# Kernel tuning notes

Hardware: AMD Instinct MI355X
Metric: run time of the kernel (lower is better)

## Reference

```python
import jax, jax.numpy as jnp
import numpy as np

B, T, D = 4, 2048, 1024
E, K, H = 8, 2, 2048

def setup_inputs() -> dict:
    key = jax.random.key(0)
    ks = jax.random.split(key, 5)
    scale = 0.02
    x = jax.random.normal(ks[0], (B, T, D), dtype=jnp.float32)
    gate_w = jax.random.normal(ks[1], (E, D), dtype=jnp.float32) * scale   # Linear(D->E) weight [out,in]
    w_gate = jax.random.normal(ks[2], (E, H, D), dtype=jnp.float32) * scale
    w_in = jax.random.normal(ks[3], (E, H, D), dtype=jnp.float32) * scale
    w_out = jax.random.normal(ks[4], (E, D, H), dtype=jnp.float32) * scale
    return {"x": x, "gate_w": gate_w, "w_gate": w_gate, "w_in": w_in, "w_out": w_out}

def reference(x, gate_w, w_gate, w_in, w_out):
    # Router: logits (B,T,E) -> top-k -> softmax over the k selected logits
    logits = jnp.einsum('btd,ed->bte', x, gate_w)
    topk_vals, topk_idx = jax.lax.top_k(logits, K)          # (B,T,K)
    routing = jax.nn.softmax(topk_vals, axis=-1)            # (B,T,K)

    out = jnp.zeros_like(x)
    # Masked-matmul: loop over the small fixed expert bank (E=8)
    for e in range(E):
        sel = (topk_idx == e)                               # (B,T,K) bool
        mask = sel.any(axis=-1)                             # (B,T)
        w = jnp.sum(routing * sel.astype(routing.dtype), axis=-1)  # (B,T)
        mx = x * mask[..., None].astype(x.dtype)            # (B,T,D)
        h = jax.nn.silu(jnp.einsum('btd,hd->bth', mx, w_gate[e])) * jnp.einsum('btd,hd->bth', mx, w_in[e])
        out = out + jnp.einsum('bth,dh->btd', h, w_out[e]) * w[..., None]
    return out
```

## Files before the change

### kernel.cpp

```cpp
#include <hip/hip_runtime.h>
#include <stdint.h>
#include <stddef.h>

#define NTOK 8192
#define DDIM 1024
#define NEXP 8
#define HDIM 2048
#define LSTRIDE (NTOK + 256)
#define NCHUNK 128
#define MAXROWS (2 * NTOK + NEXP * 256)

typedef __attribute__((ext_vector_type(4))) float f32x4;
typedef __attribute__((ext_vector_type(8))) short s16x8;
typedef __attribute__((ext_vector_type(4))) short s16x4;

static __device__ __forceinline__ unsigned short f2bf(float f) {
  union { float f; unsigned u; } v; v.f = f;
  unsigned r = v.u + 0x7FFFu + ((v.u >> 16) & 1u);
  return (unsigned short)(r >> 16);
}
static __device__ __forceinline__ float bf2f(unsigned short h) {
  union { unsigned u; float f; } v; v.u = ((unsigned)h) << 16;
  return v.f;
}

static __device__ __forceinline__ void gll16(const void* g, void* l) {
  __builtin_amdgcn_global_load_lds((const __attribute__((address_space(1))) void*)g,
                                   (__attribute__((address_space(3))) void*)l, 16, 0, 0);
}

#define BAR_MID() __builtin_amdgcn_s_barrier()
#define BAR_END() do { __builtin_amdgcn_s_barrier(); __builtin_amdgcn_sched_barrier(0); } while (0)
#define LGKM0() do { asm volatile("s_waitcnt lgkmcnt(0)" ::: "memory"); __builtin_amdgcn_sched_barrier(0); } while (0)
#define VMW6() asm volatile("s_waitcnt vmcnt(6)" ::: "memory")
#define VMW0() asm volatile("s_waitcnt vmcnt(0)" ::: "memory")

__global__ void k_sentinel(float* out) { if (threadIdx.x == 0) out[0] = 1.0e6f; }

__global__ __launch_bounds__(256) void k_cvt(const float* __restrict__ src,
                                             unsigned short* __restrict__ dst, int n8) {
  int i = blockIdx.x * blockDim.x + threadIdx.x;
  int stride = gridDim.x * blockDim.x;
  for (; i < n8; i += stride) {
    const f32x4* s = (const f32x4*)(src + (size_t)i * 8);
    f32x4 a = s[0], b = s[1];
    s16x8 o;
    o[0] = f2bf(a[0]); o[1] = f2bf(a[1]); o[2] = f2bf(a[2]); o[3] = f2bf(a[3]);
    o[4] = f2bf(b[0]); o[5] = f2bf(b[1]); o[6] = f2bf(b[2]); o[7] = f2bf(b[3]);
    *(s16x8*)(dst + (size_t)i * 8) = o;
  }
}

__global__ __launch_bounds__(256) void k_router(const float* __restrict__ x,
    const float* __restrict__ gw, unsigned* __restrict__ tokE, float2* __restrict__ tokW2,
    unsigned short* __restrict__ xbf) {
  int lane = threadIdx.x & 63;
  int t = blockIdx.x * 4 + (threadIdx.x >> 6);
  const f32x4* x4 = (const f32x4*)x;
  const f32x4* g4 = (const f32x4*)gw;
  f32x4 xr[4];
#pragma unroll
  for (int j = 0; j < 4; ++j) xr[j] = x4[(size_t)t * 256 + j * 64 + lane];
#pragma unroll
  for (int j = 0; j < 4; ++j) {
    s16x4 o;
    o[0] = f2bf(xr[j][0]); o[1] = f2bf(xr[j][1]); o[2] = f2bf(xr[j][2]); o[3] = f2bf(xr[j][3]);
    *(s16x4*)(xbf + (size_t)t * DDIM + (j * 64 + lane) * 4) = o;
  }
  float le[8];
#pragma unroll
  for (int e = 0; e < 8; ++e) {
    float p = 0.f;
#pragma unroll
    for (int j = 0; j < 4; ++j) {
      f32x4 g = g4[e * 256 + j * 64 + lane];
      p += xr[j][0] * g[0] + xr[j][1] * g[1] + xr[j][2] * g[2] + xr[j][3] * g[3];
    }
#pragma unroll
    for (int off = 32; off > 0; off >>= 1) p += __shfl_xor(p, off, 64);
    le[e] = p;
  }
  if (lane == 0) {
    int i0 = 0; float v0 = le[0];
#pragma unroll
    for (int e = 1; e < 8; ++e) if (le[e] > v0) { v0 = le[e]; i0 = e; }
    int i1 = -1; float v1 = 0.f;
#pragma unroll
    for (int e = 0; e < 8; ++e) if (e != i0 && (i1 < 0 || le[e] > v1)) { v1 = le[e]; i1 = e; }
    float b = __expf(v1 - v0);
    float s = 1.f + b;
    tokE[t] = (unsigned)i0 | ((unsigned)i1 << 8);
    tokW2[t] = make_float2(1.f / s, b / s);
  }
}

__global__ __launch_bounds__(64) void k_hist(const unsigned* __restrict__ tokE,
                                             int* __restrict__ cntTable) {
  __shared__ int c8[NEXP];
  int tid = threadIdx.x, c = blockIdx.x;
  if (tid < NEXP) c8[tid] = 0;
  __syncthreads();
  unsigned v = tokE[c * 64 + tid];
  atomicAdd(&c8[v & 255], 1);
  atomicAdd(&c8[(v >> 8) & 255], 1);
  __syncthreads();
  if (tid < NEXP) cntTable[tid * NCHUNK + c] = c8[tid];
}

__global__ __launch_bounds__(64) void k_scan(const int* __restrict__ cntTable,
                                             int* __restrict__ ctrl, int* __restrict__ cbL) {
  __shared__ int tot[NEXP];
  int e = threadIdx.x;
  if (e < NEXP) {
    int s = 0;
    for (int c = 0; c < NCHUNK; ++c) s += cntTable[e * NCHUNK + c];
    tot[e] = s; ctrl[e] = s;
  }
  __syncthreads();
  if (e == 0) {
    int acc = 0;
    for (int q = 0; q < NEXP; ++q) { ctrl[8 + q] = acc; acc += (tot[q] + 255) & ~255; }
  }
  if (e < NEXP) {
    int run = 0;
    for (int c = 0; c < NCHUNK; ++c) { cbL[e * NCHUNK + c] = run; run += cntTable[e * NCHUNK + c]; }
  }
}

__global__ __launch_bounds__(64) void k_scatter(const unsigned* __restrict__ tokE,
    const float2* __restrict__ tokW2, const int* __restrict__ cbL,
    int* __restrict__ listTok, float* __restrict__ listW, int* __restrict__ listSlot) {
  __shared__ int lcnt[NEXP];
  int tid = threadIdx.x, c = blockIdx.x;
  if (tid < NEXP) lcnt[tid] = 0;
  __syncthreads();
  int t = c * 64 + tid;
  unsigned v = tokE[t];
  int e0 = v & 255, e1 = (v >> 8) & 255;
  float2 w = tokW2[t];
  int l0 = atomicAdd(&lcnt[e0], 1);
  int l1 = atomicAdd(&lcnt[e1], 1);
  int i0 = cbL[e0 * NCHUNK + c] + l0;
  int i1 = cbL[e1 * NCHUNK + c] + l1;
  listTok[e0 * LSTRIDE + i0] = t; listW[e0 * LSTRIDE + i0] = w.x; listSlot[e0 * LSTRIDE + i0] = 0;
  listTok[e1 * LSTRIDE + i1] = t; listW[e1 * LSTRIDE + i1] = w.y; listSlot[e1 * LSTRIDE + i1] = 1;
}

__global__ __launch_bounds__(512, 2) void k_gemm1(const unsigned short* __restrict__ xbf,
    const unsigned short* __restrict__ wg, const unsigned short* __restrict__ wi,
    const int* __restrict__ ctrl, const int* __restrict__ listTok,
    unsigned short* __restrict__ hbuf) {
  int e = blockIdx.z;
  int cnt = ctrl[e];
  int m0 = blockIdx.y * 256;
  if (m0 >= cnt) return;
  int rowb = ctrl[8 + e];
  int n0 = blockIdx.x * 128;

  __shared__ __align__(16) char lds[131072];
  char* ldsc = &lds[0];

  int tid = threadIdx.x, lane = tid & 63, wv = tid >> 6;
  int wm = wv >> 1, wn = wv & 1;

  int srow = tid >> 3;
  int scol = (((tid & 7) ^ ((tid >> 3) & 7)) << 4);
  int sdst = wv << 10;
  const char* pA[2][2];
  const char* pBg[2];
  const char* pBi[2];
#pragma unroll
  for (int rg = 0; rg < 2; ++rg)
#pragma unroll
    for (int sb = 0; sb < 2; ++sb) {
      int tok = listTok[e * LSTRIDE + m0 + rg * 128 + sb * 64 + srow];
      pA[rg][sb] = (const char*)xbf + (size_t)tok * 2048 + scol;
    }
#pragma unroll
  for (int sb = 0; sb < 2; ++sb) {
    pBg[sb] = (const char*)wg + ((size_t)e * HDIM + n0 + sb * 64 + srow) * 2048 + scol;
    pBi[sb] = (const char*)wi + ((size_t)e * HDIM + n0 + sb * 64 + srow) * 2048 + scol;
  }

  int rowB = (lane & 15) << 7;
  int mk = (lane & 7) << 4;
  int q16 = (lane >> 4) << 4;
  int c0 = q16 ^ mk, c1 = (q16 + 64) ^ mk;
  int aO0 = 32768 + (wm >> 1) * 16384 + ((wm & 1) * 64) * 128 + rowB + c0;
  int aO1 = aO0 - c0 + c1;
  int gO0 = (wn * 64) * 128 + rowB + c0;
  int gO1 = gO0 - c0 + c1;
  int iO0 = 16384 + (wn * 64) * 128 + rowB + c0;
  int iO1 = iO0 - c0 + c1;

#define G1_STA(BUF, RG, KO) do { \
    gll16(pA[RG][0] + (KO), ldsc + (BUF) + 32768 + (RG) * 16384 + sdst); \
    gll16(pA[RG][1] + (KO), ldsc + (BUF) + 32768 + (RG) * 16384 + 8192 + sdst); } while (0)
#define G1_STG(BUF, KO) do { \
    gll16(pBg[0] + (KO), ldsc + (BUF) + sdst); \
    gll16(pBg[1] + (KO), ldsc + (BUF) + 8192 + sdst); } while (0)
#define G1_STI(BUF, KO) do { \
    gll16(pBi[0] + (KO), ldsc + (BUF) + 16384 + sdst); \
    gll16(pBi[1] + (KO), ldsc + (BUF) + 16384 + 8192 + sdst); } while (0)
#define G1_RDA(BUF) { _Pragma("unroll") for (int mf = 0; mf < 4; ++mf) { \
    af[mf][0] = *(const s16x8*)(ldsc + (BUF) + aO0 + mf * 2048); \
    af[mf][1] = *(const s16x8*)(ldsc + (BUF) + aO1 + mf * 2048); } }
#define G1_RDG(BUF) { _Pragma("unroll") for (int nf = 0; nf < 4; ++nf) { \
    bg[nf][0] = *(const s16x8*)(ldsc + (BUF) + gO0 + nf * 2048); \
    bg[nf][1] = *(const s16x8*)(ldsc + (BUF) + gO1 + nf * 2048); } }
#define G1_RDI(BUF) { _Pragma("unroll") for (int nf = 0; nf < 4; ++nf) { \
    bi[nf][0] = *(const s16x8*)(ldsc + (BUF) + iO0 + nf * 2048); \
    bi[nf][1] = *(const s16x8*)(ldsc + (BUF) + iO1 + nf * 2048); } }
#define G1_MMG(NH) do { __builtin_amdgcn_s_setprio(1); \
    _Pragma("unroll") for (int mf = 0; mf < 4; ++mf) _Pragma("unroll") for (int nf = 0; nf < 2; ++nf) { \
      accg[mf][(NH)*2+nf] = __builtin_amdgcn_mfma_f32_16x16x32_bf16(af[mf][0], bg[(NH)*2+nf][0], accg[mf][(NH)*2+nf], 0, 0, 0); \
      accg[mf][(NH)*2+nf] = __builtin_amdgcn_mfma_f32_16x16x32_bf16(af[mf][1], bg[(NH)*2+nf][1], accg[mf][(NH)*2+nf], 0, 0, 0); } \
    __builtin_amdgcn_s_setprio(0); } while (0)
#define G1_MMI(NH) do { __builtin_amdgcn_s_setprio(1); \
    _Pragma("unroll") for (int mf = 0; mf < 4; ++mf) _Pragma("unroll") for (int nf = 0; nf < 2; ++nf) { \
      acci[mf][(NH)*2+nf] = __builtin_amdgcn_mfma_f32_16x16x32_bf16(af[mf][0], bi[(NH)*2+nf][0], acci[mf][(NH)*2+nf], 0, 0, 0); \
      acci[mf][(NH)*2+nf] = __builtin_amdgcn_mfma_f32_16x16x32_bf16(af[mf][1], bi[(NH)*2+nf][1], acci[mf][(NH)*2+nf], 0, 0, 0); } \
    __builtin_amdgcn_s_setprio(0); } while (0)

  f32x4 accg[4][4], acci[4][4];
#pragma unroll
  for (int a = 0; a < 4; ++a)
#pragma unroll
    for (int b = 0; b < 4; ++b) { accg[a][b] = (f32x4){0.f,0.f,0.f,0.f}; acci[a][b] = (f32x4){0.f,0.f,0.f,0.f}; }
  s16x8 af[4][2], bg[4][2], bi[4][2];

  G1_STG(0, 0); G1_STA(0, 0, 0); G1_STI(0, 0); G1_STA(0, 1, 0);
  G1_STG(65536, 128); G1_STA(65536, 0, 128); G1_STI(65536, 128);
  VMW6();
  BAR_END();

  const int NIT = DDIM / 128;
  for (int i = 0; i < NIT; ++i) {
    const int koC = (2 * i + 1) * 128, koA = (2 * i + 2) * 128, koB = (2 * i + 3) * 128;
    const bool more = (i + 1 < NIT);
    G1_RDA(0); G1_RDG(0);
    G1_STA(65536, 1, koC);
    BAR_MID(); LGKM0();
    G1_MMG(0);
    BAR_END();
    if (more) G1_STG(0, koA);
    BAR_MID();
    G1_MMG(1);
    BAR_END();
    G1_RDI(0);
    if (more) G1_STA(0, 0, koA);
    BAR_MID(); LGKM0();
    G1_MMI(0);
    BAR_END();
    if (more) G1_STI(0, koA);
    BAR_MID();
    G1_MMI(1);
    if (more) VMW6(); else VMW0();
    BAR_END();
    G1_RDA(65536); G1_RDG(65536);
    if (more) G1_STA(0, 1, koA);
    BAR_MID(); LGKM0();
    G1_MMG(0);
    BAR_END();
    if (more) G1_STG(65536, koB);
    BAR_MID();
    G1_MMG(1);
    BAR_END();
    G1_RDI(65536);
    if (more) G1_STA(65536, 0, koB);
    BAR_MID(); LGKM0();
    G1_MMI(0);
    BAR_END();
    if (more) G1_STI(65536, koB);
    BAR_MID();
    G1_MMI(1);
    if (more) VMW6();
    BAR_END();
  }

#pragma unroll
  for (int mf = 0; mf < 4; ++mf)
#pragma unroll
    for (int j = 0; j < 4; ++j) {
      int r = wm * 64 + mf * 16 + ((lane >> 4) << 2) + j;
      size_t rowoff = (size_t)(rowb + m0 + r) * HDIM;
#pragma unroll
      for (int nf = 0; nf < 4; ++nf) {
        int cc = n0 + wn * 64 + nf * 16 + (lane & 15);
        float g = accg[mf][nf][j];
        float iv = acci[mf][nf][j];
        float hv = g / (1.f + __expf(-g)) * iv;
        hbuf[rowoff + cc] = f2bf(hv);
      }
    }
#undef G1_STA
#undef G1_STG
#undef G1_STI
#undef G1_RDA
#undef G1_RDG
#undef G1_RDI
#undef G1_MMG
#undef G1_MMI
}

__global__ __launch_bounds__(512, 2) void k_gemm2(const unsigned short* __restrict__ hbuf,
    const unsigned short* __restrict__ wo, const int* __restrict__ ctrl,
    const int* __restrict__ listTok, const float* __restrict__ listW,
    const int* __restrict__ listSlot, unsigned short* __restrict__ ybuf) {
  int e = blockIdx.z;
  int cnt = ctrl[e];
  int m0 = blockIdx.y * 256;
  if (m0 >= cnt) return;
  int rowb = ctrl[8 + e];
  int n0 = blockIdx.x * 256;

  __shared__ __align__(16) char lds[131072];
  char* ldsc = &lds[0];

  int tid = threadIdx.x, lane = tid & 63, wv = tid >> 6;
  int wm = wv >> 2, wn = wv & 3;

  int srow = tid >> 3;
  int scol = (((tid & 7) ^ ((tid >> 3) & 7)) << 4);
  int sdst = wv << 10;
  const char* pA[2][2];
  const char* pB[2][2];
#pragma unroll
  for (int rg = 0; rg < 2; ++rg)
#pragma unroll
    for (int sb = 0; sb < 2; ++sb) {
      int tr = rg * 128 + sb * 64 + srow;
      pA[rg][sb] = (const char*)hbuf + (size_t)(rowb + m0 + tr) * 4096 + scol;
      pB[rg][sb] = (const char*)wo + ((size_t)e * DDIM + n0 + tr) * 4096 + scol;
    }

  int rowB = (lane & 15) << 7;
  int mk = (lane & 7) << 4;
  int q16 = (lane >> 4) << 4;
  int c0 = q16 ^ mk, c1 = (q16 + 64) ^ mk;
  int aO0 = 32768 + wm * 16384 + rowB + c0;
  int aO1 = aO0 - c0 + c1;
  int bO0 = (wn >> 1) * 16384 + ((wn & 1) * 64) * 128 + rowB + c0;
  int bO1 = bO0 - c0 + c1;

#define G2_STA(BUF, RG, KO) do { \
    gll16(pA[RG][0] + (KO), ldsc + (BUF) + 32768 + (RG) * 16384 + sdst); \
    gll16(pA[RG][1] + (KO), ldsc + (BUF) + 32768 + (RG) * 16384 + 8192 + sdst); } while (0)
#define G2_STB(BUF, RG, KO) do { \
    gll16(pB[RG][0] + (KO), ldsc + (BUF) + (RG) * 16384 + sdst); \
    gll16(pB[RG][1] + (KO), ldsc + (BUF) + (RG) * 16384 + 8192 + sdst); } while (0)
#define G2_RDA(BUF, MH) { _Pragma("unroll") for (int mf = 0; mf < 4; ++mf) { \
    af[mf][0] = *(const s16x8*)(ldsc + (BUF) + aO0 + ((MH) * 64 + mf * 16) * 128); \
    af[mf][1] = *(const s16x8*)(ldsc + (BUF) + aO1 + ((MH) * 64 + mf * 16) * 128); } }
#define G2_RDB(BUF) { _Pragma("unroll") for (int nf = 0; nf < 4; ++nf) { \
    bf[nf][0] = *(const s16x8*)(ldsc + (BUF) + bO0 + nf * 2048); \
    bf[nf][1] = *(const s16x8*)(ldsc + (BUF) + bO1 + nf * 2048); } }
#define G2_MM(MH, NH) do { __builtin_amdgcn_s_setprio(1); \
    _Pragma("unroll") for (int mf = 0; mf < 4; ++mf) _Pragma("unroll") for (int nf = 0; nf < 2; ++nf) { \
      acc[(MH)*4+mf][(NH)*2+nf] = __builtin_amdgcn_mfma_f32_16x16x32_bf16(af[mf][0], bf[(NH)*2+nf][0], acc[(MH)*4+mf][(NH)*2+nf], 0, 0, 0); \
      acc[(MH)*4+mf][(NH)*2+nf] = __builtin_amdgcn_mfma_f32_16x16x32_bf16(af[mf][1], bf[(NH)*2+nf][1], acc[(MH)*4+mf][(NH)*2+nf], 0, 0, 0); } \
    __builtin_amdgcn_s_setprio(0); } while (0)

  f32x4 acc[8][4];
#pragma unroll
  for (int a = 0; a < 8; ++a)
#pragma unroll
    for (int b = 0; b < 4; ++b) acc[a][b] = (f32x4){0.f,0.f,0.f,0.f};
  s16x8 af[4][2], bf[4][2];

  G2_STB(0, 0, 0); G2_STB(0, 1, 0); G2_STA(0, 0, 0); G2_STA(0, 1, 0);
  G2_STB(65536, 0, 128); G2_STB(65536, 1, 128); G2_STA(65536, 0, 128);
  VMW6();
  BAR_END();

  const int NIT = HDIM / 128;
  for (int i = 0; i < NIT; ++i) {
    const int koC = (2 * i + 1) * 128, koA = (2 * i + 2) * 128, koB = (2 * i + 3) * 128;
    const bool more = (i + 1 < NIT);
    G2_RDA(0, 0); G2_RDB(0);
    G2_STA(65536, 1, koC);
    BAR_MID(); LGKM0();
    G2_MM(0, 0);
    BAR_END();
    if (more) G2_STB(0, 0, koA);
    BAR_MID();
    G2_MM(0, 1);
    BAR_END();
    G2_RDA(0, 1);
    if (more) G2_STB(0, 1, koA);
    BAR_MID(); LGKM0();
    G2_MM(1, 0);
    BAR_END();
    if (more) G2_STA(0, 0, koA);
    BAR_MID();
    G2_MM(1, 1);
    if (more) VMW6(); else VMW0();
    BAR_END();
    G2_RDA(65536, 0); G2_RDB(65536);
    if (more) G2_STA(0, 1, koA);
    BAR_MID(); LGKM0();
    G2_MM(0, 0);
    BAR_END();
    if (more) G2_STB(65536, 0, koB);
    BAR_MID();
    G2_MM(0, 1);
    BAR_END();
    G2_RDA(65536, 1);
    if (more) G2_STB(65536, 1, koB);
    BAR_MID(); LGKM0();
    G2_MM(1, 0);
    BAR_END();
    if (more) G2_STA(65536, 0, koB);
    BAR_MID();
    G2_MM(1, 1);
    if (more) VMW6();
    BAR_END();
  }

#pragma unroll
  for (int mf = 0; mf < 8; ++mf)
#pragma unroll
    for (int j = 0; j < 4; ++j) {
      int r = wm * 128 + mf * 16 + ((lane >> 4) << 2) + j;
      int mrow = m0 + r;
      if (mrow < cnt) {
        int tok = listTok[e * LSTRIDE + mrow];
        float wgt = listW[e * LSTRIDE + mrow];
        int slot = listSlot[e * LSTRIDE + mrow];
        size_t base = ((size_t)slot * NTOK + tok) * DDIM + n0 + wn * 64;
#pragma unroll
        for (int nf = 0; nf < 4; ++nf)
          ybuf[base + nf * 16 + (lane & 15)] = f2bf(acc[mf][nf][j] * wgt);
      }
    }
#undef G2_STA
#undef G2_STB
#undef G2_RDA
#undef G2_RDB
#undef G2_MM
}

__global__ __launch_bounds__(256) void k_reduce(const unsigned short* __restrict__ ybuf,
                                                float* __restrict__ out, int n8) {
  int i = blockIdx.x * blockDim.x + threadIdx.x;
  int stride = gridDim.x * blockDim.x;
  const unsigned short* y0 = ybuf;
  const unsigned short* y1 = ybuf + (size_t)NTOK * DDIM;
  for (; i < n8; i += stride) {
    s16x8 a = *(const s16x8*)(y0 + (size_t)i * 8);
    s16x8 b = *(const s16x8*)(y1 + (size_t)i * 8);
    f32x4 o0, o1;
#pragma unroll
    for (int j = 0; j < 4; ++j) o0[j] = bf2f((unsigned short)a[j]) + bf2f((unsigned short)b[j]);
#pragma unroll
    for (int j = 0; j < 4; ++j) o1[j] = bf2f((unsigned short)a[4 + j]) + bf2f((unsigned short)b[4 + j]);
    f32x4* d = (f32x4*)(out + (size_t)i * 8);
    d[0] = o0; d[1] = o1;
  }
}

extern "C" void kernel_launch(void* const* d_in, const int* in_sizes, int n_in,
                              void* d_out, int out_size, void* d_ws, size_t ws_size,
                              hipStream_t stream) {
  const float* x     = (const float*)d_in[0];
  const float* gw    = (const float*)d_in[1];
  const float* wgate = (const float*)d_in[2];
  const float* win   = (const float*)d_in[3];
  const float* wout  = (const float*)d_in[4];
  float* out = (float*)d_out;

  const size_t LBYTES     = (size_t)NEXP * LSTRIDE * 4;
  const size_t OFF_LIST   = 256;
  const size_t OFF_LISTW  = OFF_LIST + LBYTES;
  const size_t ZERO_BYTES = OFF_LISTW;
  const size_t OFF_SLOT   = OFF_LISTW + LBYTES;
  const size_t OFF_CB     = OFF_SLOT + LBYTES;
  const size_t OFF_CT     = OFF_CB + 4096;
  const size_t OFF_TE     = OFF_CT + 4096;
  const size_t OFF_TW     = OFF_TE + (size_t)NTOK * 4;
  const size_t OFF_XBF = (size_t)1 << 20;
  const size_t OFF_WG  = OFF_XBF + (size_t)NTOK * DDIM * 2;
  const size_t OFF_WI  = OFF_WG + (size_t)NEXP * HDIM * DDIM * 2;
  const size_t OFF_WO  = OFF_WI + (size_t)NEXP * HDIM * DDIM * 2;
  const size_t OFF_H   = OFF_WO + (size_t)NEXP * DDIM * HDIM * 2;
  const size_t OFF_Y   = OFF_WG;
  const size_t TOTAL   = OFF_H + (size_t)MAXROWS * HDIM * 2;

  if (ws_size < TOTAL) { k_sentinel<<<1, 64, 0, stream>>>(out); return; }

  char* ws = (char*)d_ws;
  int* ctrl            = (int*)ws;
  int* listTok         = (int*)(ws + OFF_LIST);
  float* listW         = (float*)(ws + OFF_LISTW);
  int* listSlot        = (int*)(ws + OFF_SLOT);
  int* cbL             = (int*)(ws + OFF_CB);
  int* cntTable        = (int*)(ws + OFF_CT);
  unsigned* tokE       = (unsigned*)(ws + OFF_TE);
  float2* tokW2        = (float2*)(ws + OFF_TW);
  unsigned short* xbf  = (unsigned short*)(ws + OFF_XBF);
  unsigned short* wgb  = (unsigned short*)(ws + OFF_WG);
  unsigned short* wib  = (unsigned short*)(ws + OFF_WI);
  unsigned short* wob  = (unsigned short*)(ws + OFF_WO);
  unsigned short* hbuf = (unsigned short*)(ws + OFF_H);
  unsigned short* ybuf = (unsigned short*)(ws + OFF_Y);

  hipMemsetAsync(ws, 0, ZERO_BYTES, stream);

  k_router<<<NTOK / 4, 256, 0, stream>>>(x, gw, tokE, tokW2, xbf);
  k_hist<<<NCHUNK, 64, 0, stream>>>(tokE, cntTable);
  k_scan<<<1, 64, 0, stream>>>(cntTable, ctrl, cbL);
  k_scatter<<<NCHUNK, 64, 0, stream>>>(tokE, tokW2, cbL, listTok, listW, listSlot);

  k_cvt<<<2048, 256, 0, stream>>>(wgate, wgb, NEXP * HDIM * DDIM / 8);
  k_cvt<<<2048, 256, 0, stream>>>(win,   wib, NEXP * HDIM * DDIM / 8);
  k_cvt<<<2048, 256, 0, stream>>>(wout,  wob, NEXP * DDIM * HDIM / 8);

  k_gemm1<<<dim3(HDIM / 128, NTOK / 256, NEXP), 512, 0, stream>>>(xbf, wgb, wib, ctrl, listTok, hbuf);
  k_gemm2<<<dim3(DDIM / 256, NTOK / 256, NEXP), 512, 0, stream>>>(hbuf, wob, ctrl, listTok, listW, listSlot, ybuf);
  k_reduce<<<2048, 256, 0, stream>>>(ybuf, out, NTOK * DDIM / 8);
}
```

Baseline: 367.2 us.

## Switch expert GEMMs to 32x32x16 MFMA and fuse weight conversion into router

Both expert GEMM kernels now use 32x32x16 bf16 MFMA tiles instead of 16x16x32. The LDS fragment addressing, accumulator layout and epilogue row mapping are rewritten to match. Larger MFMA tiles issue fewer instructions and need fewer LDS fragment reads per unit of work. Separately, the three weight fp32-to-bf16 conversion launches are merged into the router kernel as extra blocks, cutting launches and letting conversion run alongside routing. The risks are errors in the new swizzled fragment indexing and different register pressure.

New measurement: 410.6 us. +11.8%, slower.

```diff
diff --git a/kernel.cpp b/kernel.cpp
--- a/kernel.cpp
+++ b/kernel.cpp
@@ -11,6 +11,7 @@
 #define MAXROWS (2 * NTOK + NEXP * 256)
 
 typedef __attribute__((ext_vector_type(4))) float f32x4;
+typedef __attribute__((ext_vector_type(16))) float f32x16;
 typedef __attribute__((ext_vector_type(8))) short s16x8;
 typedef __attribute__((ext_vector_type(4))) short s16x4;
 
@@ -37,25 +38,33 @@
 
 __global__ void k_sentinel(float* out) { if (threadIdx.x == 0) out[0] = 1.0e6f; }
 
-__global__ __launch_bounds__(256) void k_cvt(const float* __restrict__ src,
-                                             unsigned short* __restrict__ dst, int n8) {
-  int i = blockIdx.x * blockDim.x + threadIdx.x;
-  int stride = gridDim.x * blockDim.x;
-  for (; i < n8; i += stride) {
-    const f32x4* s = (const f32x4*)(src + (size_t)i * 8);
-    f32x4 a = s[0], b = s[1];
-    s16x8 o;
-    o[0] = f2bf(a[0]); o[1] = f2bf(a[1]); o[2] = f2bf(a[2]); o[3] = f2bf(a[3]);
-    o[4] = f2bf(b[0]); o[5] = f2bf(b[1]); o[6] = f2bf(b[2]); o[7] = f2bf(b[3]);
-    *(s16x8*)(dst + (size_t)i * 8) = o;
-  }
-}
-
-__global__ __launch_bounds__(256) void k_router(const float* __restrict__ x,
-    const float* __restrict__ gw, unsigned* __restrict__ tokE, float2* __restrict__ tokW2,
-    unsigned short* __restrict__ xbf) {
+__global__ __launch_bounds__(256) void k_prep(const float* __restrict__ x,
+    const float* __restrict__ gw,
+    const float* __restrict__ wgate, const float* __restrict__ win, const float* __restrict__ wout,
+    unsigned short* __restrict__ wgb, unsigned short* __restrict__ wib, unsigned short* __restrict__ wob,
+    unsigned* __restrict__ tokE, float2* __restrict__ tokW2, unsigned short* __restrict__ xbf) {
+  int b = blockIdx.x;
+  if (b >= 2048) {
+    const float* srcs[3] = { wgate, win, wout };
+    unsigned short* dsts[3] = { wgb, wib, wob };
+    int g = (b - 2048) * 256 + threadIdx.x;
+    const int stride = 1536 * 256;
+#pragma unroll
+    for (int it = 0; it < 16; ++it) {
+      int arr = g >> 21;
+      int idx = g & ((1 << 21) - 1);
+      const f32x4* s = (const f32x4*)(srcs[arr] + (size_t)idx * 8);
+      f32x4 a = s[0], c = s[1];
+      s16x8 o;
+      o[0] = f2bf(a[0]); o[1] = f2bf(a[1]); o[2] = f2bf(a[2]); o[3] = f2bf(a[3]);
+      o[4] = f2bf(c[0]); o[5] = f2bf(c[1]); o[6] = f2bf(c[2]); o[7] = f2bf(c[3]);
+      *(s16x8*)(dsts[arr] + (size_t)idx * 8) = o;
+      g += stride;
+    }
+    return;
+  }
   int lane = threadIdx.x & 63;
-  int t = blockIdx.x * 4 + (threadIdx.x >> 6);
+  int t = b * 4 + (threadIdx.x >> 6);
   const f32x4* x4 = (const f32x4*)x;
   const f32x4* g4 = (const f32x4*)gw;
   f32x4 xr[4];
@@ -87,10 +96,10 @@
     int i1 = -1; float v1 = 0.f;
 #pragma unroll
     for (int e = 0; e < 8; ++e) if (e != i0 && (i1 < 0 || le[e] > v1)) { v1 = le[e]; i1 = e; }
-    float b = __expf(v1 - v0);
-    float s = 1.f + b;
+    float bb = __expf(v1 - v0);
+    float s = 1.f + bb;
     tokE[t] = (unsigned)i0 | ((unsigned)i1 << 8);
-    tokW2[t] = make_float2(1.f / s, b / s);
+    tokW2[t] = make_float2(1.f / s, bb / s);
   }
 }
 
@@ -182,16 +191,15 @@
     pBi[sb] = (const char*)wi + ((size_t)e * HDIM + n0 + sb * 64 + srow) * 2048 + scol;
   }
 
-  int rowB = (lane & 15) << 7;
+  int rowB = (lane & 31) << 7;
   int mk = (lane & 7) << 4;
-  int q16 = (lane >> 4) << 4;
-  int c0 = q16 ^ mk, c1 = (q16 + 64) ^ mk;
-  int aO0 = 32768 + (wm >> 1) * 16384 + ((wm & 1) * 64) * 128 + rowB + c0;
-  int aO1 = aO0 - c0 + c1;
-  int gO0 = (wn * 64) * 128 + rowB + c0;
-  int gO1 = gO0 - c0 + c1;
-  int iO0 = 16384 + (wn * 64) * 128 + rowB + c0;
-  int iO1 = iO0 - c0 + c1;
+  int kg = (lane >> 5) << 4;
+  int cs[4];
+#pragma unroll
+  for (int s = 0; s < 4; ++s) cs[s] = (s * 32 + kg) ^ mk;
+  int aBase = 32768 + (wm >> 1) * 16384 + ((wm & 1) * 64) * 128 + rowB;
+  int gBase = (wn * 64) * 128 + rowB;
+  int iBase = 16384 + (wn * 64) * 128 + rowB;
 
 #define G1_STA(BUF, RG, KO) do { \
     gll16(pA[RG][0] + (KO), ldsc + (BUF) + 32768 + (RG) * 16384 + sdst); \
@@ -202,32 +210,32 @@
 #define G1_STI(BUF, KO) do { \
     gll16(pBi[0] + (KO), ldsc + (BUF) + 16384 + sdst); \
     gll16(pBi[1] + (KO), ldsc + (BUF) + 16384 + 8192 + sdst); } while (0)
-#define G1_RDA(BUF) { _Pragma("unroll") for (int mf = 0; mf < 4; ++mf) { \
-    af[mf][0] = *(const s16x8*)(ldsc + (BUF) + aO0 + mf * 2048); \
-    af[mf][1] = *(const s16x8*)(ldsc + (BUF) + aO1 + mf * 2048); } }
-#define G1_RDG(BUF) { _Pragma("unroll") for (int nf = 0; nf < 4; ++nf) { \
-    bg[nf][0] = *(const s16x8*)(ldsc + (BUF) + gO0 + nf * 2048); \
-    bg[nf][1] = *(const s16x8*)(ldsc + (BUF) + gO1 + nf * 2048); } }
-#define G1_RDI(BUF) { _Pragma("unroll") for (int nf = 0; nf < 4; ++nf) { \
-    bi[nf][0] = *(const s16x8*)(ldsc + (BUF) + iO0 + nf * 2048); \
-    bi[nf][1] = *(const s16x8*)(ldsc + (BUF) + iO1 + nf * 2048); } }
-#define G1_MMG(NH) do { __builtin_amdgcn_s_setprio(1); \
-    _Pragma("unroll") for (int mf = 0; mf < 4; ++mf) _Pragma("unroll") for (int nf = 0; nf < 2; ++nf) { \
-      accg[mf][(NH)*2+nf] = __builtin_amdgcn_mfma_f32_16x16x32_bf16(af[mf][0], bg[(NH)*2+nf][0], accg[mf][(NH)*2+nf], 0, 0, 0); \
-      accg[mf][(NH)*2+nf] = __builtin_amdgcn_mfma_f32_16x16x32_bf16(af[mf][1], bg[(NH)*2+nf][1], accg[mf][(NH)*2+nf], 0, 0, 0); } \
+#define G1_RDA(BUF) { _Pragma("unroll") for (int mf = 0; mf < 2; ++mf) _Pragma("unroll") for (int s = 0; s < 4; ++s) \
+    af[mf][s] = *(const s16x8*)(ldsc + (BUF) + aBase + mf * 4096 + cs[s]); }
+#define G1_RDG(BUF) { _Pragma("unroll") for (int nf = 0; nf < 2; ++nf) _Pragma("unroll") for (int s = 0; s < 4; ++s) \
+    bg[nf][s] = *(const s16x8*)(ldsc + (BUF) + gBase + nf * 4096 + cs[s]); }
+#define G1_RDI(BUF) { _Pragma("unroll") for (int nf = 0; nf < 2; ++nf) _Pragma("unroll") for (int s = 0; s < 4; ++s) \
+    bi[nf][s] = *(const s16x8*)(ldsc + (BUF) + iBase + nf * 4096 + cs[s]); }
+#define G1_MMG(SH) do { __builtin_amdgcn_s_setprio(1); \
+    _Pragma("unroll") for (int mf = 0; mf < 2; ++mf) _Pragma("unroll") for (int nf = 0; nf < 2; ++nf) { \
+      accg[mf][nf] = __builtin_amdgcn_mfma_f32_32x32x16_bf16(af[mf][(SH)*2], bg[nf][(SH)*2], accg[mf][nf], 0, 0, 0); \
+      accg[mf][nf] = __builtin_amdgcn_mfma_f32_32x32x16_bf16(af[mf][(SH)*2+1], bg[nf][(SH)*2+1], accg[mf][nf], 0, 0, 0); } \
     __builtin_amdgcn_s_setprio(0); } while (0)
-#define G1_MMI(NH) do { __builtin_amdgcn_s_setprio(1); \
-    _Pragma("unroll") for (int mf = 0; mf < 4; ++mf) _Pragma("unroll") for (int nf = 0; nf < 2; ++nf) { \
-      acci[mf][(NH)*2+nf] = __builtin_amdgcn_mfma_f32_16x16x32_bf16(af[mf][0], bi[(NH)*2+nf][0], acci[mf][(NH)*2+nf], 0, 0, 0); \
-      acci[mf][(NH)*2+nf] = __builtin_amdgcn_mfma_f32_16x16x32_bf16(af[mf][1], bi[(NH)*2+nf][1], acci[mf][(NH)*2+nf], 0, 0, 0); } \
+#define G1_MMI(SH) do { __builtin_amdgcn_s_setprio(1); \
+    _Pragma("unroll") for (int mf = 0; mf < 2; ++mf) _Pragma("unroll") for (int nf = 0; nf < 2; ++nf) { \
+      acci[mf][nf] = __builtin_amdgcn_mfma_f32_32x32x16_bf16(af[mf][(SH)*2], bi[nf][(SH)*2], acci[mf][nf], 0, 0, 0); \
+      acci[mf][nf] = __builtin_amdgcn_mfma_f32_32x32x16_bf16(af[mf][(SH)*2+1], bi[nf][(SH)*2+1], acci[mf][nf], 0, 0, 0); } \
     __builtin_amdgcn_s_setprio(0); } while (0)
 
-  f32x4 accg[4][4], acci[4][4];
-#pragma unroll
-  for (int a = 0; a < 4; ++a)
-#pragma unroll
-    for (int b = 0; b < 4; ++b) { accg[a][b] = (f32x4){0.f,0.f,0.f,0.f}; acci[a][b] = (f32x4){0.f,0.f,0.f,0.f}; }
-  s16x8 af[4][2], bg[4][2], bi[4][2];
+  f32x16 accg[2][2], acci[2][2];
+#pragma unroll
+  for (int a = 0; a < 2; ++a)
+#pragma unroll
+    for (int b = 0; b < 2; ++b) {
+#pragma unroll
+      for (int q = 0; q < 16; ++q) { accg[a][b][q] = 0.f; acci[a][b][q] = 0.f; }
+    }
+  s16x8 af[2][4], bg[2][4], bi[2][4];
 
   G1_STG(0, 0); G1_STA(0, 0, 0); G1_STI(0, 0); G1_STA(0, 1, 0);
   G1_STG(65536, 128); G1_STA(65536, 0, 128); G1_STI(65536, 128);
@@ -279,16 +287,16 @@
   }
 
 #pragma unroll
-  for (int mf = 0; mf < 4; ++mf)
-#pragma unroll
-    for (int j = 0; j < 4; ++j) {
-      int r = wm * 64 + mf * 16 + ((lane >> 4) << 2) + j;
-      size_t rowoff = (size_t)(rowb + m0 + r) * HDIM;
-#pragma unroll
-      for (int nf = 0; nf < 4; ++nf) {
-        int cc = n0 + wn * 64 + nf * 16 + (lane & 15);
-        float g = accg[mf][nf][j];
-        float iv = acci[mf][nf][j];
+  for (int mf = 0; mf < 2; ++mf)
+#pragma unroll
+    for (int r = 0; r < 16; ++r) {
+      int row = wm * 64 + mf * 32 + (r & 3) + 8 * (r >> 2) + 4 * (lane >> 5);
+      size_t rowoff = (size_t)(rowb + m0 + row) * HDIM;
+#pragma unroll
+      for (int nf = 0; nf < 2; ++nf) {
+        int cc = n0 + wn * 64 + nf * 32 + (lane & 31);
+        float g = accg[mf][nf][r];
+        float iv = acci[mf][nf][r];
         float hv = g / (1.f + __expf(-g)) * iv;
         hbuf[rowoff + cc] = f2bf(hv);
       }
@@ -334,14 +342,14 @@
       pB[rg][sb] = (const char*)wo + ((size_t)e * DDIM + n0 + tr) * 4096 + scol;
     }
 
-  int rowB = (lane & 15) << 7;
+  int rowB = (lane & 31) << 7;
   int mk = (lane & 7) << 4;
-  int q16 = (lane >> 4) << 4;
-  int c0 = q16 ^ mk, c1 = (q16 + 64) ^ mk;
-  int aO0 = 32768 + wm * 16384 + rowB + c0;
-  int aO1 = aO0 - c0 + c1;
-  int bO0 = (wn >> 1) * 16384 + ((wn & 1) * 64) * 128 + rowB + c0;
-  int bO1 = bO0 - c0 + c1;
+  int kg = (lane >> 5) << 4;
+  int cs[4];
+#pragma unroll
+  for (int s = 0; s < 4; ++s) cs[s] = (s * 32 + kg) ^ mk;
+  int aBase = 32768 + wm * 16384 + rowB;
+  int bBase = (wn >> 1) * 16384 + ((wn & 1) * 64) * 128 + rowB;
 
 #define G2_STA(BUF, RG, KO) do { \
     gll16(pA[RG][0] + (KO), ldsc + (BUF) + 32768 + (RG) * 16384 + sdst); \
@@ -349,24 +357,25 @@
 #define G2_STB(BUF, RG, KO) do { \
     gll16(pB[RG][0] + (KO), ldsc + (BUF) + (RG) * 16384 + sdst); \
     gll16(pB[RG][1] + (KO), ldsc + (BUF) + (RG) * 16384 + 8192 + sdst); } while (0)
-#define G2_RDA(BUF, MH) { _Pragma("unroll") for (int mf = 0; mf < 4; ++mf) { \
-    af[mf][0] = *(const s16x8*)(ldsc + (BUF) + aO0 + ((MH) * 64 + mf * 16) * 128); \
-    af[mf][1] = *(const s16x8*)(ldsc + (BUF) + aO1 + ((MH) * 64 + mf * 16) * 128); } }
-#define G2_RDB(BUF) { _Pragma("unroll") for (int nf = 0; nf < 4; ++nf) { \
-    bf[nf][0] = *(const s16x8*)(ldsc + (BUF) + bO0 + nf * 2048); \
-    bf[nf][1] = *(const s16x8*)(ldsc + (BUF) + bO1 + nf * 2048); } }
-#define G2_MM(MH, NH) do { __builtin_amdgcn_s_setprio(1); \
-    _Pragma("unroll") for (int mf = 0; mf < 4; ++mf) _Pragma("unroll") for (int nf = 0; nf < 2; ++nf) { \
-      acc[(MH)*4+mf][(NH)*2+nf] = __builtin_amdgcn_mfma_f32_16x16x32_bf16(af[mf][0], bf[(NH)*2+nf][0], acc[(MH)*4+mf][(NH)*2+nf], 0, 0, 0); \
-      acc[(MH)*4+mf][(NH)*2+nf] = __builtin_amdgcn_mfma_f32_16x16x32_bf16(af[mf][1], bf[(NH)*2+nf][1], acc[(MH)*4+mf][(NH)*2+nf], 0, 0, 0); } \
+#define G2_RDA(BUF, MH) { _Pragma("unroll") for (int m2 = 0; m2 < 2; ++m2) _Pragma("unroll") for (int s = 0; s < 4; ++s) \
+    af[m2][s] = *(const s16x8*)(ldsc + (BUF) + aBase + ((MH) * 2 + m2) * 4096 + cs[s]); }
+#define G2_RDB(BUF) { _Pragma("unroll") for (int nf = 0; nf < 2; ++nf) _Pragma("unroll") for (int s = 0; s < 4; ++s) \
+    bf[nf][s] = *(const s16x8*)(ldsc + (BUF) + bBase + nf * 4096 + cs[s]); }
+#define G2_MM(MH, SH) do { __builtin_amdgcn_s_setprio(1); \
+    _Pragma("unroll") for (int m2 = 0; m2 < 2; ++m2) _Pragma("unroll") for (int nf = 0; nf < 2; ++nf) { \
+      acc[(MH)*2+m2][nf] = __builtin_amdgcn_mfma_f32_32x32x16_bf16(af[m2][(SH)*2], bf[nf][(SH)*2], acc[(MH)*2+m2][nf], 0, 0, 0); \
+      acc[(MH)*2+m2][nf] = __builtin_amdgcn_mfma_f32_32x32x16_bf16(af[m2][(SH)*2+1], bf[nf][(SH)*2+1], acc[(MH)*2+m2][nf], 0, 0, 0); } \
     __builtin_amdgcn_s_setprio(0); } while (0)
 
-  f32x4 acc[8][4];
-#pragma unroll
-  for (int a = 0; a < 8; ++a)
-#pragma unroll
-    for (int b = 0; b < 4; ++b) acc[a][b] = (f32x4){0.f,0.f,0.f,0.f};
-  s16x8 af[4][2], bf[4][2];
+  f32x16 acc[4][2];
+#pragma unroll
+  for (int a = 0; a < 4; ++a)
+#pragma unroll
+    for (int b = 0; b < 2; ++b) {
+#pragma unroll
+      for (int q = 0; q < 16; ++q) acc[a][b][q] = 0.f;
+    }
+  s16x8 af[2][4], bf[2][4];
 
   G2_STB(0, 0, 0); G2_STB(0, 1, 0); G2_STA(0, 0, 0); G2_STA(0, 1, 0);
   G2_STB(65536, 0, 128); G2_STB(65536, 1, 128); G2_STA(65536, 0, 128);
@@ -418,19 +427,19 @@
   }
 
 #pragma unroll
-  for (int mf = 0; mf < 8; ++mf)
-#pragma unroll
-    for (int j = 0; j < 4; ++j) {
-      int r = wm * 128 + mf * 16 + ((lane >> 4) << 2) + j;
-      int mrow = m0 + r;
+  for (int mf = 0; mf < 4; ++mf)
+#pragma unroll
+    for (int r = 0; r < 16; ++r) {
+      int row = wm * 128 + mf * 32 + (r & 3) + 8 * (r >> 2) + 4 * (lane >> 5);
+      int mrow = m0 + row;
       if (mrow < cnt) {
         int tok = listTok[e * LSTRIDE + mrow];
         float wgt = listW[e * LSTRIDE + mrow];
         int slot = listSlot[e * LSTRIDE + mrow];
         size_t base = ((size_t)slot * NTOK + tok) * DDIM + n0 + wn * 64;
 #pragma unroll
-        for (int nf = 0; nf < 4; ++nf)
-          ybuf[base + nf * 16 + (lane & 15)] = f2bf(acc[mf][nf][j] * wgt);
+        for (int nf = 0; nf < 2; ++nf)
+          ybuf[base + nf * 32 + (lane & 31)] = f2bf(acc[mf][nf][r] * wgt);
       }
     }
 #undef G2_STA
@@ -506,15 +515,11 @@
 
   hipMemsetAsync(ws, 0, ZERO_BYTES, stream);
 
-  k_router<<<NTOK / 4, 256, 0, stream>>>(x, gw, tokE, tokW2, xbf);
+  k_prep<<<3584, 256, 0, stream>>>(x, gw, wgate, win, wout, wgb, wib, wob, tokE, tokW2, xbf);
   k_hist<<<NCHUNK, 64, 0, stream>>>(tokE, cntTable);
   k_scan<<<1, 64, 0, stream>>>(cntTable, ctrl, cbL);
   k_scatter<<<NCHUNK, 64, 0, stream>>>(tokE, tokW2, cbL, listTok, listW, listSlot);
 
-  k_cvt<<<2048, 256, 0, stream>>>(wgate, wgb, NEXP * HDIM * DDIM / 8);
-  k_cvt<<<2048, 256, 0, stream>>>(win,   wib, NEXP * HDIM * DDIM / 8);
-  k_cvt<<<2048, 256, 0, stream>>>(wout,  wob, NEXP * DDIM * HDIM / 8);
-
   k_gemm1<<<dim3(HDIM / 128, NTOK / 256, NEXP), 512, 0, stream>>>(xbf, wgb, wib, ctrl, listTok, hbuf);
   k_gemm2<<<dim3(DDIM / 256, NTOK / 256, NEXP), 512, 0, stream>>>(hbuf, wob, ctrl, listTok, listW, listSlot, ybuf);
   k_reduce<<<2048, 256, 0, stream>>>(ybuf, out, NTOK * DDIM / 8);
```

## Fuse router with weight conversion and swizzle GEMM block order for XCD locality

Applied to the files above, without the earlier changes.

Merges the router and the three fp32-to-bf16 weight conversion kernels into one launch, with extra blocks doing the conversion. Remaps the grouped GEMM grids to 1D with a swizzle so consecutive block IDs on the same XCD share an expert and M tile, improving L2 reuse of activations and weights. The reduce launch uses fewer blocks. This trades some mapping arithmetic and a fixed unrolled conversion loop for fewer launches and better cache locality.

Result: slower. 405.7 us (+10.5%).

```diff
diff --git a/kernel.cpp b/kernel.cpp
--- a/kernel.cpp
+++ b/kernel.cpp
@@ -37,25 +37,33 @@
 
 __global__ void k_sentinel(float* out) { if (threadIdx.x == 0) out[0] = 1.0e6f; }
 
-__global__ __launch_bounds__(256) void k_cvt(const float* __restrict__ src,
-                                             unsigned short* __restrict__ dst, int n8) {
-  int i = blockIdx.x * blockDim.x + threadIdx.x;
-  int stride = gridDim.x * blockDim.x;
-  for (; i < n8; i += stride) {
-    const f32x4* s = (const f32x4*)(src + (size_t)i * 8);
-    f32x4 a = s[0], b = s[1];
-    s16x8 o;
-    o[0] = f2bf(a[0]); o[1] = f2bf(a[1]); o[2] = f2bf(a[2]); o[3] = f2bf(a[3]);
-    o[4] = f2bf(b[0]); o[5] = f2bf(b[1]); o[6] = f2bf(b[2]); o[7] = f2bf(b[3]);
-    *(s16x8*)(dst + (size_t)i * 8) = o;
-  }
-}
-
-__global__ __launch_bounds__(256) void k_router(const float* __restrict__ x,
-    const float* __restrict__ gw, unsigned* __restrict__ tokE, float2* __restrict__ tokW2,
-    unsigned short* __restrict__ xbf) {
+__global__ __launch_bounds__(256) void k_prep(const float* __restrict__ x,
+    const float* __restrict__ gw,
+    const float* __restrict__ wgate, const float* __restrict__ win, const float* __restrict__ wout,
+    unsigned short* __restrict__ wgb, unsigned short* __restrict__ wib, unsigned short* __restrict__ wob,
+    unsigned* __restrict__ tokE, float2* __restrict__ tokW2, unsigned short* __restrict__ xbf) {
+  int b = blockIdx.x;
+  if (b >= 2048) {
+    const float* srcs[3] = { wgate, win, wout };
+    unsigned short* dsts[3] = { wgb, wib, wob };
+    int g = (b - 2048) * 256 + threadIdx.x;
+    const int stride = 1536 * 256;
+#pragma unroll
+    for (int it = 0; it < 16; ++it) {
+      int arr = g >> 21;
+      int idx = g & ((1 << 21) - 1);
+      const f32x4* s = (const f32x4*)(srcs[arr] + (size_t)idx * 8);
+      f32x4 a = s[0], c = s[1];
+      s16x8 o;
+      o[0] = f2bf(a[0]); o[1] = f2bf(a[1]); o[2] = f2bf(a[2]); o[3] = f2bf(a[3]);
+      o[4] = f2bf(c[0]); o[5] = f2bf(c[1]); o[6] = f2bf(c[2]); o[7] = f2bf(c[3]);
+      *(s16x8*)(dsts[arr] + (size_t)idx * 8) = o;
+      g += stride;
+    }
+    return;
+  }
   int lane = threadIdx.x & 63;
-  int t = blockIdx.x * 4 + (threadIdx.x >> 6);
+  int t = b * 4 + (threadIdx.x >> 6);
   const f32x4* x4 = (const f32x4*)x;
   const f32x4* g4 = (const f32x4*)gw;
   f32x4 xr[4];
@@ -87,10 +95,10 @@
     int i1 = -1; float v1 = 0.f;
 #pragma unroll
     for (int e = 0; e < 8; ++e) if (e != i0 && (i1 < 0 || le[e] > v1)) { v1 = le[e]; i1 = e; }
-    float b = __expf(v1 - v0);
-    float s = 1.f + b;
+    float bb = __expf(v1 - v0);
+    float s = 1.f + bb;
     tokE[t] = (unsigned)i0 | ((unsigned)i1 << 8);
-    tokW2[t] = make_float2(1.f / s, b / s);
+    tokW2[t] = make_float2(1.f / s, bb / s);
   }
 }
 
@@ -150,12 +158,16 @@
     const unsigned short* __restrict__ wg, const unsigned short* __restrict__ wi,
     const int* __restrict__ ctrl, const int* __restrict__ listTok,
     unsigned short* __restrict__ hbuf) {
-  int e = blockIdx.z;
+  int bid = blockIdx.x;
+  int xc = bid & 7, w = bid >> 3;
+  int nb = w & 15;
+  int p = ((w >> 4) << 3) | xc;
+  int m = p & 31, e = p >> 5;
   int cnt = ctrl[e];
-  int m0 = blockIdx.y * 256;
+  int m0 = m << 8;
   if (m0 >= cnt) return;
   int rowb = ctrl[8 + e];
-  int n0 = blockIdx.x * 128;
+  int n0 = nb << 7;
 
   __shared__ __align__(16) char lds[131072];
   char* ldsc = &lds[0];
@@ -307,12 +319,16 @@
     const unsigned short* __restrict__ wo, const int* __restrict__ ctrl,
     const int* __restrict__ listTok, const float* __restrict__ listW,
     const int* __restrict__ listSlot, unsigned short* __restrict__ ybuf) {
-  int e = blockIdx.z;
+  int bid = blockIdx.x;
+  int xc = bid & 7, w = bid >> 3;
+  int nb = w & 3;
+  int p = ((w >> 2) << 3) | xc;
+  int m = p & 31, e = p >> 5;
   int cnt = ctrl[e];
-  int m0 = blockIdx.y * 256;
+  int m0 = m << 8;
   if (m0 >= cnt) return;
   int rowb = ctrl[8 + e];
-  int n0 = blockIdx.x * 256;
+  int n0 = nb << 8;
 
   __shared__ __align__(16) char lds[131072];
   char* ldsc = &lds[0];
@@ -506,16 +522,12 @@
 
   hipMemsetAsync(ws, 0, ZERO_BYTES, stream);
 
-  k_router<<<NTOK / 4, 256, 0, stream>>>(x, gw, tokE, tokW2, xbf);
+  k_prep<<<3584, 256, 0, stream>>>(x, gw, wgate, win, wout, wgb, wib, wob, tokE, tokW2, xbf);
   k_hist<<<NCHUNK, 64, 0, stream>>>(tokE, cntTable);
   k_scan<<<1, 64, 0, stream>>>(cntTable, ctrl, cbL);
   k_scatter<<<NCHUNK, 64, 0, stream>>>(tokE, tokW2, cbL, listTok, listW, listSlot);
 
-  k_cvt<<<2048, 256, 0, stream>>>(wgate, wgb, NEXP * HDIM * DDIM / 8);
-  k_cvt<<<2048, 256, 0, stream>>>(win,   wib, NEXP * HDIM * DDIM / 8);
-  k_cvt<<<2048, 256, 0, stream>>>(wout,  wob, NEXP * DDIM * HDIM / 8);
-
-  k_gemm1<<<dim3(HDIM / 128, NTOK / 256, NEXP), 512, 0, stream>>>(xbf, wgb, wib, ctrl, listTok, hbuf);
-  k_gemm2<<<dim3(DDIM / 256, NTOK / 256, NEXP), 512, 0, stream>>>(hbuf, wob, ctrl, listTok, listW, listSlot, ybuf);
-  k_reduce<<<2048, 256, 0, stream>>>(ybuf, out, NTOK * DDIM / 8);
-}
+  k_gemm1<<<16 * 32 * NEXP, 512, 0, stream>>>(xbf, wgb, wib, ctrl, listTok, hbuf);
+  k_gemm2<<<4 * 32 * NEXP, 512, 0, stream>>>(hbuf, wob, ctrl, listTok, listW, listSlot, ybuf);
+  k_reduce<<<512, 256, 0, stream>>>(ybuf, out, NTOK * DDIM / 8);
+}
```
